# Kernel optimization log

Hardware: AMD Instinct MI355X
Metric: run time of the kernel (lower is better)

Reference implementation:

```python
import jax, jax.numpy as jnp
import numpy as np
from jax.scipy.special import gammaln

EPS = 1e-8
N_SAMPLES = 2 ** 17
ATTACK_FULL_SIZE = 2048
CPD = 16
N_RES = 16
EXPR = 2
N_OSC = 2
N_GAUSS = 8
N_EVENTS = 4
FRAMES = 128
DEF_FRAMES = 128
N_LEVELS = 11  # log2(ATTACK_FULL_SIZE)


def unit_norm(x, axis=-1):
    return x / (jnp.linalg.norm(x, axis=axis, keepdims=True) + EPS)


def fft_convolve(a, b):
    # zero-pad to 2n to avoid circular wraparound, multiply spectra, crop to n
    n = a.shape[-1]
    fa = jnp.fft.rfft(a, n=2 * n, axis=-1)
    fb = jnp.fft.rfft(b, n=2 * n, axis=-1)
    return jnp.fft.irfft(fa * fb, n=2 * n, axis=-1)[..., :n]


def upsample_with_holes(x, size):
    # zero-insertion upsampling: place frames at stride `factor`
    factor = size // x.shape[-1]
    out = jnp.zeros(x.shape[:-1] + (size,), x.dtype)
    return out.at[..., ::factor].set(x)


def interpolate_last_axis(x, size):
    # linear interpolation, align_corners=False semantics (torch F.interpolate)
    n = x.shape[-1]
    scale = n / size
    src = jnp.clip((jnp.arange(size) + 0.5) * scale - 0.5, 0.0, n - 1.0)
    lo = jnp.floor(src).astype(jnp.int32)
    hi = jnp.minimum(lo + 1, n - 1)
    w = (src - lo).astype(x.dtype)
    return x[..., lo] * (1.0 - w) + x[..., hi] * w


def ensure_last_axis_length(x, size):
    n = x.shape[-1]
    if n == size:
        return x
    if n > size:
        return x[..., :size]
    return jnp.pad(x, [(0, 0)] * (x.ndim - 1) + [(0, size - n)])


def sparse_softmax(x):
    # hard one-hot forward, softmax straight-through backward
    sm = jax.nn.softmax(x, axis=-1)
    hard = jax.nn.one_hot(jnp.argmax(x, axis=-1), x.shape[-1], dtype=x.dtype)
    return hard + sm - jax.lax.stop_gradient(sm)


def hierarchical_dirac(p):
    # p: (..., L, 2) binary choices per level -> one-hot dirac of length 2**L
    sel = sparse_softmax(p)
    sig = sel[..., 0, :]
    for i in range(1, p.shape[-2]):
        sig = (sig[..., :, None] * sel[..., i, :][..., None, :]).reshape(*sig.shape[:-1], -1)
    return sig


def gamma_pdf(mean, std, n_elements):
    # gamma pdf on support (eps, 1], parameterized by mean/std
    t = jnp.linspace(EPS, 1.0, n_elements)
    k = (mean / (std + EPS)) ** 2
    rate = mean / (std ** 2 + EPS)
    k = k[..., None]
    rate = rate[..., None]
    logp = k * jnp.log(rate + EPS) + (k - 1.0) * jnp.log(t) - rate * t - gammaln(k)
    return jnp.exp(logp)


def damped_harmonic_oscillator(time, mass, damping, tension, x0):
    # underdamped closed-form solution, v0 = 0
    omega0_sq = tension / mass
    gamma = damping / (2.0 * mass)
    omega = jnp.sqrt(omega0_sq - gamma ** 2)
    A = x0
    B = gamma * x0 / omega
    return jnp.exp(-gamma * time) * (A * jnp.cos(omega * time) + B * jnp.sin(omega * time))


def dho_block(damping, mass, tension, disp, amps, tmod=None, scaling=None):
    time = jnp.linspace(0.0, 10.0, N_SAMPLES).reshape(1, 1, 1, N_SAMPLES)
    t = tension[..., None]  # (N_OSC, N_RES, EXPR, 1)
    if tmod is not None:
        t = t + tmod[0] * scaling  # broadcast -> (N_OSC, N_RES, EXPR, N_SAMPLES)
    x = damped_harmonic_oscillator(
        time,
        jax.nn.sigmoid(mass[..., None]) * 2.0,
        jax.nn.sigmoid(damping[..., None]) * 30.0,
        10.0 ** t,
        disp[..., None],
    )
    x = (x * amps).sum(axis=0)  # sum over oscillators
    return x.reshape(1, 1, N_RES, EXPR, N_SAMPLES)


def attack_envelopes(means, stds, amps, pos, overall_amp):
    m, s, a = jnp.abs(means), jnp.abs(stds), jnp.abs(amps)
    p = hierarchical_dirac(pos)  # (1,1,CPD,NG,2048)
    x = gamma_pdf(m, s, ATTACK_FULL_SIZE) * a[..., None]
    x = fft_convolve(x, p)
    x = x.sum(axis=2)  # (1,1,NG,2048)
    x = unit_norm(x)
    x = x * overall_amp[..., None]  # broadcast -> (1,1,CPD,NG,2048)
    x = x.sum(axis=-2)  # (1,1,CPD,2048)
    return x.reshape(CPD, ATTACK_FULL_SIZE)


def _forward(control_signal, deformations, ae_means, ae_stds, ae_amps, ae_pos,
             ae_overall_amp, dho_damping, dho_mass, dho_tension, dho_disp, dho_amp,
             influences, stack_mix, router, layer_mix, gains, attack_noise):
    b, ne, cpd, frames = control_signal.shape
    # --- DampedHarmonicOscillatorStack ---
    o1 = dho_block(dho_damping[0], dho_mass[0], dho_tension[0], dho_disp[0], dho_amp[0])
    o2 = dho_block(dho_damping[1], dho_mass[1], dho_tension[1], dho_disp[1], dho_amp[1], o1, influences[0])
    o3 = dho_block(dho_damping[2], dho_mass[2], dho_tension[2], dho_disp[2], dho_amp[2], o2, influences[1])
    res = (jnp.stack([o1, o2, o3], axis=-1) * jax.nn.softmax(stack_mix, axis=-1)).sum(axis=-1)
    res = unit_norm(res)
    # --- AttackEnvelopes ---
    ae = attack_envelopes(ae_means, ae_stds, ae_amps, ae_pos, ae_overall_amp)
    # --- execute_layer ---
    routed = jnp.einsum('becf,cr->berf', control_signal, router)
    before = routed
    res = unit_norm(res)  # execute_layer normalizes again
    routed = upsample_with_holes(routed.reshape(b, ne, N_RES, 1, frames), N_SAMPLES)
    # ae.shape[-1] == window_size, so materialize_attack_envelopes just multiplies noise
    impulse = ensure_last_axis_length(ae * attack_noise, N_SAMPLES).reshape(1, 1, cpd, 1, N_SAMPLES)
    routed = fft_convolve(impulse, routed)  # (1,ne,N_RES,1,S)
    cs = routed.reshape(1, ne, cpd, N_SAMPLES).sum(axis=1, keepdims=True)
    conv = fft_convolve(routed, res)  # (1,ne,N_RES,EXPR,S)
    base = jnp.zeros_like(deformations).at[:, :, 0:1, :].set(1.0)
    d = jax.nn.softmax(base + deformations, axis=-2)
    d = interpolate_last_axis(d.reshape(b, 1, 1, EXPR, -1), N_SAMPLES)
    x = (d * conv).sum(axis=-2)  # (1,ne,N_RES,S)
    mixes = jax.nn.softmax(layer_mix.reshape(1, 1, N_RES, 1, 1, 2), axis=-1)
    stacked = jnp.stack([routed, x.reshape(routed.shape)], axis=-1)
    x = (mixes * stacked).sum(axis=-1)
    x = x.reshape(1, 1, N_RES, -1)
    summed = jnp.tanh(x * jnp.abs(gains.reshape(1, 1, N_RES, 1)))
    summed = summed.sum(axis=-2, keepdims=True)
    return summed, before, cs


def setup_inputs() -> dict:
    key = jax.random.key(0)
    ks = jax.random.split(key, 20)
    u = lambda k, shape, lo, hi: jax.random.uniform(k, shape, jnp.float32, lo, hi)
    inp = {}
    inp['control_signal'] = jax.random.uniform(ks[0], (1, N_EVENTS, CPD, FRAMES), jnp.float32)
    inp['deformations'] = jax.random.normal(ks[1], (1, 1, EXPR, DEF_FRAMES), jnp.float32)
    inp['ae_means'] = u(ks[2], (1, 1, CPD, N_GAUSS), -6.0, 6.0)
    inp['ae_stds'] = u(ks[3], (1, 1, CPD, N_GAUSS), 0.5, 6.0)
    inp['ae_amps'] = u(ks[4], (1, 1, CPD, N_GAUSS), -6.0, 6.0)
    inp['ae_pos'] = u(ks[5], (1, 1, CPD, N_GAUSS, N_LEVELS, 2), -1.0, 1.0)
    inp['ae_overall_amp'] = u(ks[6], (1, 1, CPD, 1), -1.0, 1.0)
    inp['dho_damping'] = u(ks[7], (3, N_OSC, N_RES, EXPR), 0.5, 1.5)
    inp['dho_mass'] = u(ks[8], (3, N_OSC, N_RES, EXPR), -2.0, 2.0)
    inp['dho_tension'] = u(ks[9], (3, N_OSC, N_RES, EXPR), 4.0, 9.0)
    inp['dho_disp'] = u(ks[10], (3, N_OSC, N_RES, EXPR), -1.0, 2.0)
    inp['dho_amp'] = u(ks[11], (3, N_OSC, N_RES, EXPR, 1), -1.0, 1.0)
    inp['influences'] = u(ks[12], (2, N_OSC, N_RES, EXPR, 1), -0.01, 0.01)
    inp['stack_mix'] = u(ks[13], (1, 1, N_RES, EXPR, 1, 3), -1.0, 1.0)
    router = u(ks[14], (CPD, N_RES), -1.0, 1.0)
    mask = (jax.random.uniform(ks[15], (CPD, N_RES)) < 0.1).astype(jnp.float32)
    inp['router'] = router * mask
    inp['layer_mix'] = u(ks[16], (N_RES, 2), -1.0, 1.0)
    inp['gains'] = u(ks[17], (N_RES, 1), 0.01, 1.1)
    inp['attack_noise'] = u(ks[18], (CPD, ATTACK_FULL_SIZE), -1.0, 1.0)
    return inp


def reference(control_signal, deformations, ae_means, ae_stds, ae_amps, ae_pos,
              ae_overall_amp, dho_damping, dho_mass, dho_tension, dho_disp, dho_amp,
              influences, stack_mix, router, layer_mix, gains, attack_noise):
    return _forward(control_signal, deformations, ae_means, ae_stds, ae_amps, ae_pos,
                    ae_overall_amp, dho_damping, dho_mass, dho_tension, dho_disp, dho_amp,
                    influences, stack_mix, router, layer_mix, gains, attack_noise)
```

## Files before the change

### kernel.cpp

```cpp
#include <hip/hip_runtime.h>
#include <math.h>

#define NS 131072
#define EPSF 1e-8f

#define OFF_IMP    8388608u
#define OFF_VG     8421376u
#define OFF_DW     8437760u
#define OFF_FV     8568832u
#define OFF_NORM   8577024u
#define OFF_MIX0   8577064u
#define OFF_MIX1   8577080u
#define OFF_GABS   8577096u
#define OFF_PART   8578560u
#define OFF_GSSP   8594944u
#define OFF_DHP    8595200u

#define AFRAG_USH  4194304u
#define ABF2_USH   4726784u
#define HB_USH     8388608u

typedef __attribute__((ext_vector_type(8))) short short8;
typedef __attribute__((ext_vector_type(4))) float floatx4;
typedef __attribute__((ext_vector_type(4))) unsigned short ushort4v;

#define INV2PI 0.15915494309189535f

__device__ __forceinline__ float sigmf(float x) { return 1.0f / (1.0f + expf(-x)); }

__device__ __forceinline__ unsigned short f2bf(float x) {
  unsigned u = __float_as_uint(x);
  unsigned r = (u + 0x7FFFu + ((u >> 16) & 1u)) >> 16;
  return (unsigned short)r;
}

__global__ __launch_bounds__(256) void k0_params(
    const float* __restrict__ ddmp, const float* __restrict__ dmas,
    const float* __restrict__ dten, const float* __restrict__ ddisp,
    const float* __restrict__ damp, const float* __restrict__ infl,
    const float* __restrict__ smix, float* __restrict__ wsf)
{
  int tid = threadIdx.x;
  int rx = tid >> 3, ent = tid & 7;
  int r = rx >> 1, x = rx & 1;
  float* g = wsf + OFF_DHP + rx * 40;
  if (ent < 6) {
    int bb = ent >> 1, o = ent & 1;
    int id = ((bb * 2 + o) * 16 + r) * 2 + x;
    float mass = 2.0f * sigmf(dmas[id]);
    float gam = 30.0f * sigmf(ddmp[id]) / (2.0f * mass);
    double W = exp((double)dten[id] * 2.302585092994046) / (double)mass;
    float x0v = ddisp[id];
    float ampv = damp[id];
    float infv = 0.f;
    if (bb == 1) infv = infl[(o * 16 + r) * 2 + x];
    if (bb == 2) infv = infl[((2 + o) * 16 + r) * 2 + x];
    g[0 + ent]  = -gam;
    g[6 + ent]  = ampv * x0v;
    g[12 + ent] = gam * ampv * x0v;
    g[18 + ent] = infv * 2.3025851f;
    if (bb == 0) {
      double om = sqrt(W - (double)gam * (double)gam);
      g[24 + o] = (float)((double)(gam * x0v * ampv) / om);
      g[26 + o] = (float)(om * 0.15915494309189535);
    } else {
      g[28 + ent - 2] = (float)W;
    }
    if (ent == 0) { g[32] = 0.f; g[36] = 0.f; g[37] = 0.f; g[38] = 0.f; g[39] = 0.f; }
  } else if (ent == 6) {
    float a0 = smix[rx * 3], a1 = smix[rx * 3 + 1], a2 = smix[rx * 3 + 2];
    float mm = fmaxf(a0, fmaxf(a1, a2));
    float e0 = expf(a0 - mm), e1 = expf(a1 - mm), e2 = expf(a2 - mm);
    float inv = 1.0f / (e0 + e1 + e2);
    g[33] = e0 * inv; g[34] = e1 * inv; g[35] = e2 * inv;
  }
}

__global__ __launch_bounds__(256) void k01_prep_dho(
    const float* __restrict__ csig, const float* __restrict__ deform,
    const float* __restrict__ smix_unused, const float* __restrict__ router,
    const float* __restrict__ lmix, const float* __restrict__ gains,
    const float* __restrict__ means, const float* __restrict__ stds,
    const float* __restrict__ amps, const float* __restrict__ pos,
    float* __restrict__ wsf, unsigned short* __restrict__ abf2,
    unsigned short* __restrict__ resb, float* __restrict__ partials,
    float* __restrict__ out)
{
  int tid = threadIdx.x;
  int bid = blockIdx.x;
  if (bid < 512) {
    int t = bid * 256 + tid;
    {
      float src = (t + 0.5f) * (1.0f / 1024.0f) - 0.5f;
      src = fminf(fmaxf(src, 0.0f), 127.0f);
      int lo = (int)src;
      int hi = min(lo + 1, 127);
      float w = src - (float)lo;
      float c0l = 1.0f / (1.0f + expf(deform[128 + lo] - (1.0f + deform[lo])));
      float c0h = 1.0f / (1.0f + expf(deform[128 + hi] - (1.0f + deform[hi])));
      wsf[OFF_DW + t] = c0l * (1.0f - w) + c0h * w;
    }
    int mt = bid & 7, e = (bid >> 3) & 3, r = (bid >> 5) & 15;
    __shared__ float fvrow[128];
    if (tid < 128) {
      float s = 0.f;
      for (int c = 0; c < 16; ++c)
        s += csig[(e * 16 + c) * 128 + tid] * router[c * 16 + r];
      fvrow[tid] = s;
      if (mt == 0) {
        wsf[OFF_FV + (e * 16 + r) * 128 + tid] = s;
        out[524288 + (e * 16 + r) * 128 + tid] = s;
      }
    }
    __syncthreads();
    {
      int gid = bid * 256 + tid;
      int lane = gid & 63;
      int kt = (gid >> 6) & 3;
      int m = lane & 15, quad = lane >> 4;
      int base = mt * 16 + m - kt * 32 - quad * 8;
      short8 v;
#pragma unroll
      for (int j = 0; j < 8; ++j) {
        int f = base - j;
        unsigned short b = 0;
        if (f >= 0 && f < 128) b = f2bf(fvrow[f]);
        v[j] = (short)b;
      }
      *(short8*)&abf2[(size_t)gid * 8] = v;
    }
    if (bid == 0 && tid < 16) {
      int r2 = tid;
      float l0 = lmix[r2 * 2], l1 = lmix[r2 * 2 + 1];
      float mx = fmaxf(l0, l1);
      float e0 = expf(l0 - mx), e1 = expf(l1 - mx), inv = 1.0f / (e0 + e1);
      wsf[OFF_MIX0 + r2] = e0 * inv;
      wsf[OFF_MIX1 + r2] = e1 * inv;
      wsf[OFF_GABS + r2] = fabsf(gains[r2]);
    }
  } else if (bid < 576) {
    int gb = bid - 512;
    int g = gb >> 3;
    int i = (gb & 7) * 256 + tid;
    __shared__ float kS[16], rateS[16], logAS[16], aS[16];
    __shared__ int dS[16];
    __shared__ float red[4];
    if (tid < 16) {
      int c = tid, idx = c * 8 + g;
      double m = fabs((double)means[idx]);
      double s = fabs((double)stds[idx]);
      double k = m / (s + 1e-8); k = k * k;
      double rate = m / (s * s + 1e-8);
      double logA = k * log(rate + 1e-8) - lgamma(k);
      kS[c] = (float)k; rateS[c] = (float)rate; logAS[c] = (float)logA;
      aS[c] = fabsf(amps[idx]);
      int d = 0;
      for (int l = 0; l < 11; ++l) {
        float p0 = pos[(idx * 11 + l) * 2], p1 = pos[(idx * 11 + l) * 2 + 1];
        d = d * 2 + (p1 > p0 ? 1 : 0);
      }
      dS[c] = d;
    }
    __syncthreads();
    const float step = (float)((1.0 - 1e-8) / 2047.0);
    float v = 0.f;
    for (int c = 0; c < 16; ++c) {
      int mi = i - dS[c];
      if (mi >= 0) {
        float tm = 1e-8f + (float)mi * step;
        float lp = logAS[c] + (kS[c] - 1.0f) * __logf(tm) - rateS[c] * tm;
        v += aS[c] * __expf(lp);
      }
    }
    wsf[OFF_VG + g * 2048 + i] = v;
    float sumsq = v * v;
#pragma unroll
    for (int off = 32; off; off >>= 1) sumsq += __shfl_down(sumsq, off, 64);
    if ((tid & 63) == 0) red[tid >> 6] = sumsq;
    __syncthreads();
    if (tid == 0) wsf[OFF_GSSP + gb] = red[0] + red[1] + red[2] + red[3];
  } else {
    int b = bid - 576;
    int rx = b >> 7;
    int t0 = (b & 127) * 1024 + tid * 4;
    __shared__ float pf[40];
    __shared__ float bred[4];
    if (tid < 40) pf[tid] = wsf[OFF_DHP + rx * 40 + tid];
    __syncthreads();
    float sqacc = 0.f;
    unsigned short h4[4];
#pragma unroll
    for (int u = 0; u < 4; ++u) {
      float ttf = (float)(t0 + u) * (10.0f / 131071.0f);
      float o1v = 0.f;
#pragma unroll
      for (int o = 0; o < 2; ++o) {
        float fr = pf[26 + o] * ttf;
        fr -= rintf(fr);
        float sn = __builtin_amdgcn_sinf(fr);
        float cn = __builtin_amdgcn_cosf(fr);
        float ex = __expf(pf[o] * ttf);
        o1v += ex * (pf[6 + o] * cn + pf[24 + o] * sn);
      }
      float prev = o1v, o2v = 0.f, o3v = 0.f;
#pragma unroll
      for (int blk = 1; blk < 3; ++blk) {
        float acc = 0.f;
#pragma unroll
        for (int oo = 0; oo < 2; ++oo) {
          int o = blk * 2 + oo;
          float ng = pf[o];
          float p10 = __expf(prev * pf[18 + o]);
          float rad = __builtin_fmaf(pf[28 + o - 2], p10, -(ng * ng));
          float om = __builtin_amdgcn_sqrtf(rad);
          float fr = (om * INV2PI) * ttf;
          fr -= rintf(fr);
          float sn = __builtin_amdgcn_sinf(fr);
          float cn = __builtin_amdgcn_cosf(fr);
          float Bp = pf[12 + o] * __builtin_amdgcn_rcpf(om);
          float ex = __expf(ng * ttf);
          acc += ex * (pf[6 + o] * cn + Bp * sn);
        }
        if (blk == 1) o2v = acc; else o3v = acc;
        prev = acc;
      }
      float rv = pf[33] * o1v + pf[34] * o2v + pf[35] * o3v;
      h4[u] = f2bf(rv);
      sqacc += rv * rv;
    }
    ushort4v hv;
    hv[0] = h4[0]; hv[1] = h4[1]; hv[2] = h4[2]; hv[3] = h4[3];
    *(ushort4v*)&resb[(size_t)rx * NS + t0] = hv;
#pragma unroll
    for (int off = 32; off; off >>= 1) sqacc += __shfl_down(sqacc, off, 64);
    if ((tid & 63) == 0) bred[tid >> 6] = sqacc;
    __syncthreads();
    if (tid == 0)
      partials[rx * 512 + (b & 127)] = bred[0] + bred[1] + bred[2] + bred[3];
  }
}

__global__ __launch_bounds__(256) void kB_mid(
    const float* __restrict__ ovamp, const float* __restrict__ noise,
    float* __restrict__ wsf, unsigned short* __restrict__ abf)
{
  int bid = blockIdx.x;
  int tid = threadIdx.x;
  if (bid < 32) {
    int rx = bid;
    const float* partials = wsf + OFF_PART;
    __shared__ float red[4];
    float s = (tid < 128) ? partials[rx * 512 + tid] : 0.f;
#pragma unroll
    for (int off = 32; off; off >>= 1) s += __shfl_down(s, off, 64);
    if ((tid & 63) == 0) red[tid >> 6] = s;
    __syncthreads();
    if (tid == 0) wsf[OFF_NORM + rx] = red[0] + red[1] + red[2] + red[3];
    return;
  }
  __shared__ float wS[8];
  if (tid < 8) {
    float g8 = 0.f;
#pragma unroll
    for (int u = 0; u < 8; ++u) g8 += wsf[OFF_GSSP + tid * 8 + u];
    wS[tid] = 1.0f / (sqrtf(g8) + EPSF);
  }
  __syncthreads();
  const float* vg = wsf + OFF_VG;
  if (bid < 160) {
    int idx0 = bid - 32;
    int c = idx0 >> 3;
    int i = (idx0 & 7) * 256 + tid;
    float S = 0.f;
#pragma unroll
    for (int g = 0; g < 8; ++g) S += vg[g * 2048 + i] * wS[g];
    wsf[OFF_IMP + c * 2048 + i] = ovamp[c] * S * noise[c * 2048 + i];
    return;
  }
  int gid = (bid - 160) * 256 + tid;
  if (gid >= 66560) return;
  int r = gid / (65 * 64);
  int rem = gid % (65 * 64);
  int sc = rem >> 6, lane = rem & 63;
  int m = lane & 15, quad = lane >> 4;
  int qp = (quad < 2) ? quad : quad - 4;
  int base = 32 * sc + m - 8 * qp;
  float oa = ovamp[r];
  short8 v;
#pragma unroll
  for (int j = 0; j < 8; ++j) {
    int idx = base - j;
    unsigned short b = 0;
    if (idx >= 0 && idx < 2048) {
      float S = 0.f;
#pragma unroll
      for (int g = 0; g < 8; ++g) S += vg[g * 2048 + idx] * wS[g];
      b = f2bf(oa * S * noise[r * 2048 + idx]);
    }
    v[j] = (short)b;
  }
  *(short8*)&abf[(size_t)gid * 8] = v;
}

__global__ __launch_bounds__(256) void k4_mfma(
    const unsigned short* __restrict__ resb, const unsigned short* __restrict__ abf,
    const float* __restrict__ wsf, unsigned short* __restrict__ Hb)
{
  int rx = blockIdx.y, r = rx >> 1;
  int n0 = blockIdx.x * 256;
  __shared__ __align__(16) unsigned short Xs[9280];
  int tid = threadIdx.x;
  for (int i = tid; i < 772; i += 256) {
    int q_rel = i >> 1, p8 = (i & 1) * 8;
    int q = n0 - 130 + q_rel;
    short8 v = {0, 0, 0, 0, 0, 0, 0, 0};
    if (q >= 0) v = *(const short8*)&resb[(size_t)rx * NS + q * 16 + p8];
    *(short8*)&Xs[q_rel * 24 + p8] = v;
  }
  __syncthreads();
  int lane = tid & 63, w = tid >> 6;
  int quad = lane >> 4, nl = lane & 15;
  float n1 = sqrtf(wsf[OFF_NORM + rx]);
  float s1 = 1.0f / (n1 + EPSF);
  float scale = s1 * (1.0f / (n1 * s1 + EPSF)) * wsf[OFF_MIX1 + r];
  const short8* af = (const short8*)(abf) + (size_t)r * 65 * 64 + lane;
  floatx4 acc0 = {0,0,0,0}, acc1 = {0,0,0,0}, acc2 = {0,0,0,0}, acc3 = {0,0,0,0};
  const char* xbase = (const char*)Xs + (size_t)(130 + w * 64 + nl - (quad >> 1)) * 48
                      + (quad & 1) * 16;
  short8 wbuf[25];
#pragma unroll
  for (int s = -24; s < 0; ++s)
    wbuf[s + 25] = *(const short8*)(xbase - 96 * s);
#pragma unroll
  for (int sc = 0; sc < 65; ++sc) {
    wbuf[sc % 25] = *(const short8*)(xbase - 96 * sc);
    short8 a = af[sc * 64];
    acc0 = __builtin_amdgcn_mfma_f32_16x16x32_bf16(a, wbuf[sc % 25],        acc0, 0, 0, 0);
    acc1 = __builtin_amdgcn_mfma_f32_16x16x32_bf16(a, wbuf[(sc + 17) % 25], acc1, 0, 0, 0);
    acc2 = __builtin_amdgcn_mfma_f32_16x16x32_bf16(a, wbuf[(sc + 9) % 25],  acc2, 0, 0, 0);
    acc3 = __builtin_amdgcn_mfma_f32_16x16x32_bf16(a, wbuf[(sc + 1) % 25],  acc3, 0, 0, 0);
  }
  unsigned short* hp = Hb + (size_t)rx * NS + 16 * (n0 + w * 64 + nl) + quad * 4;
  ushort4v h0, h1, h2, h3;
#pragma unroll
  for (int i = 0; i < 4; ++i) {
    h0[i] = f2bf(acc0[i] * scale);
    h1[i] = f2bf(acc1[i] * scale);
    h2[i] = f2bf(acc2[i] * scale);
    h3[i] = f2bf(acc3[i] * scale);
  }
  *(ushort4v*)(hp)       = h0;
  *(ushort4v*)(hp + 256) = h1;
  *(ushort4v*)(hp + 512) = h2;
  *(ushort4v*)(hp + 768) = h3;
}

__global__ __launch_bounds__(256) void k6_mfma(
    const unsigned short* __restrict__ Hb, const float* __restrict__ imp,
    const unsigned short* __restrict__ abf2,
    const float* __restrict__ wsf, float* __restrict__ out)
{
  int rm = blockIdx.y;
  int n0 = blockIdx.x * 16;
  int zz = blockIdx.z;
  int tid = threadIdx.x;
  int wm = tid >> 6, lane = tid & 63;
  int quad = lane >> 4, n = lane & 15;
  int col = n0 + n;
  int mt = zz * 4 + wm;

  __shared__ float fvs2[4][4][128];
  for (int i = tid; i < 2048; i += 256) {
    int rq = i >> 9, e = (i >> 7) & 3, q = i & 127;
    fvs2[rq][e][q] = wsf[OFF_FV + (e * 16 + rq * 4 + rm) * 128 + q];
  }
  __syncthreads();

  float d0r[4];
  const float* dwg = wsf + OFF_DW;
#pragma unroll
  for (int i = 0; i < 4; ++i) {
    int q = mt * 16 + quad * 4 + i;
    d0r[i] = dwg[q * 1024 + col];
  }

  float tansum[4] = {0.f, 0.f, 0.f, 0.f};
  const short8* af = (const short8*)abf2;

  for (int rq = 0; rq < 4; ++rq) {
    int r = rq * 4 + rm;
    short8 bf0[4], bf1[4];
    const unsigned short* H0 = Hb + (size_t)(2 * r) * NS + col;
    const unsigned short* H1 = Hb + (size_t)(2 * r + 1) * NS + col;
#pragma unroll
    for (int kt = 0; kt < 4; ++kt) {
#pragma unroll
      for (int j = 0; j < 8; ++j) {
        int p = kt * 32 + quad * 8 + j;
        bf0[kt][j] = (short)H0[(size_t)p * 1024];
        bf1[kt][j] = (short)H1[(size_t)p * 1024];
      }
    }
    float impA = imp[r * 2048 + col];
    float impB = imp[r * 2048 + 1024 + col];
    float mix0r = wsf[OFF_MIX0 + r];
    float csum[4] = {0.f, 0.f, 0.f, 0.f};

    for (int e = 0; e < 4; ++e) {
      float ge = wsf[OFF_GABS + 4 * e + rq];
      const short8* afe = af + ((size_t)(r * 4 + e) * 32) * 64 + lane;
      floatx4 acc0 = {0, 0, 0, 0}, acc1 = {0, 0, 0, 0};
#pragma unroll
      for (int kt = 0; kt < 4; ++kt) {
        short8 a = afe[(mt * 4 + kt) * 64];
        acc0 = __builtin_amdgcn_mfma_f32_16x16x32_bf16(a, bf0[kt], acc0, 0, 0, 0);
        acc1 = __builtin_amdgcn_mfma_f32_16x16x32_bf16(a, bf1[kt], acc1, 0, 0, 0);
      }
#pragma unroll
      for (int i = 0; i < 4; ++i) {
        int q = mt * 16 + quad * 4 + i;
        float fq = fvs2[rq][e][q];
        float fqm = (q > 0) ? fvs2[rq][e][q - 1] : 0.f;
        float rsv = fq * impA + fqm * impB;
        csum[i] += rsv;
        float d0 = d0r[i];
        float conv = d0 * acc0[i] + (1.0f - d0) * acc1[i];
        float z = (mix0r * rsv + conv) * ge;
        float e2 = __expf(2.0f * z);
        tansum[i] += 1.0f - 2.0f * __builtin_amdgcn_rcpf(e2 + 1.0f);
      }
    }
#pragma unroll
    for (int i = 0; i < 4; ++i) {
      int q = mt * 16 + quad * 4 + i;
      out[532480 + (size_t)r * NS + q * 1024 + col] = csum[i];
    }
  }
#pragma unroll
  for (int i = 0; i < 4; ++i) {
    int q = mt * 16 + quad * 4 + i;
    out[(size_t)rm * NS + q * 1024 + col] = tansum[i];
  }
}

extern "C" void kernel_launch(void* const* d_in, const int* in_sizes, int n_in,
                              void* d_out, int out_size, void* d_ws, size_t ws_size,
                              hipStream_t stream) {
  const float* csig   = (const float*)d_in[0];
  const float* deform = (const float*)d_in[1];
  const float* aem    = (const float*)d_in[2];
  const float* aes    = (const float*)d_in[3];
  const float* aea    = (const float*)d_in[4];
  const float* aep    = (const float*)d_in[5];
  const float* aeo    = (const float*)d_in[6];
  const float* ddmp   = (const float*)d_in[7];
  const float* dmas   = (const float*)d_in[8];
  const float* dten   = (const float*)d_in[9];
  const float* ddisp  = (const float*)d_in[10];
  const float* damp   = (const float*)d_in[11];
  const float* infl   = (const float*)d_in[12];
  const float* smix   = (const float*)d_in[13];
  const float* router = (const float*)d_in[14];
  const float* lmix   = (const float*)d_in[15];
  const float* gains  = (const float*)d_in[16];
  const float* anoise = (const float*)d_in[17];

  float*  wsf = (float*)d_ws;
  unsigned short* resb = (unsigned short*)d_ws;
  unsigned short* abf  = (unsigned short*)d_ws + AFRAG_USH;
  unsigned short* abf2 = (unsigned short*)d_ws + ABF2_USH;
  unsigned short* Hb   = (unsigned short*)d_ws + HB_USH;
  float*  out = (float*)d_out;

  k0_params<<<1, 256, 0, stream>>>(ddmp, dmas, dten, ddisp, damp, infl, smix, wsf);
  k01_prep_dho<<<4672, 256, 0, stream>>>(csig, deform, smix, router, lmix, gains,
                                         aem, aes, aea, aep, wsf, abf2, resb,
                                         wsf + OFF_PART, out);
  kB_mid<<<420, 256, 0, stream>>>(aeo, anoise, wsf, abf);
  k4_mfma<<<dim3(32, 32), 256, 0, stream>>>(resb, abf, wsf, Hb);
  k6_mfma<<<dim3(64, 4, 2), 256, 0, stream>>>(Hb, wsf + OFF_IMP, abf2, wsf, out);
}
```

Baseline: 163.0 us.

## Use rotation recurrence for DHO oscillators, 8 samples per thread, vectorize attack frags

Each thread in the DHO phase of the prep kernel now computes 8 consecutive samples instead of 4. The fixed-frequency first oscillator's sin/cos and all damping exponentials are advanced by multiplying with per-step rotation and decay factors precomputed in the params kernel, so per-sample transcendentals are no longer needed for those terms. Block count and the partials reduction are adjusted to match. The bf16 attack-fragment builder in kB_mid gains a fast path that does vectorized unaligned float4 loads for interior indices. The recurrence can accumulate float rounding drift over the 8 steps.

Result: no change. 161.8 us, median of 2 (-0.7%).

```diff
diff --git a/kernel.cpp b/kernel.cpp
--- a/kernel.cpp
+++ b/kernel.cpp
@@ -23,6 +23,7 @@
 typedef __attribute__((ext_vector_type(8))) short short8;
 typedef __attribute__((ext_vector_type(4))) float floatx4;
 typedef __attribute__((ext_vector_type(4))) unsigned short ushort4v;
+typedef __attribute__((ext_vector_type(4), aligned(4))) float float4u;
 
 #define INV2PI 0.15915494309189535f
 
@@ -43,7 +44,8 @@
   int tid = threadIdx.x;
   int rx = tid >> 3, ent = tid & 7;
   int r = rx >> 1, x = rx & 1;
-  float* g = wsf + OFF_DHP + rx * 40;
+  float* g = wsf + OFF_DHP + rx * 48;
+  const double dtd = 10.0 / 131071.0;
   if (ent < 6) {
     int bb = ent >> 1, o = ent & 1;
     int id = ((bb * 2 + o) * 16 + r) * 2 + x;
@@ -59,14 +61,17 @@
     g[6 + ent]  = ampv * x0v;
     g[12 + ent] = gam * ampv * x0v;
     g[18 + ent] = infv * 2.3025851f;
+    g[40 + ent] = (float)exp(-(double)gam * dtd);
     if (bb == 0) {
       double om = sqrt(W - (double)gam * (double)gam);
       g[24 + o] = (float)((double)(gam * x0v * ampv) / om);
       g[26 + o] = (float)(om * 0.15915494309189535);
+      g[36 + o] = (float)sin(om * dtd);
+      g[38 + o] = (float)cos(om * dtd);
     } else {
       g[28 + ent - 2] = (float)W;
     }
-    if (ent == 0) { g[32] = 0.f; g[36] = 0.f; g[37] = 0.f; g[38] = 0.f; g[39] = 0.f; }
+    if (ent == 0) { g[32] = 0.f; g[46] = 0.f; g[47] = 0.f; }
   } else if (ent == 6) {
     float a0 = smix[rx * 3], a1 = smix[rx * 3 + 1], a2 = smix[rx * 3 + 2];
     float mm = fmaxf(a0, fmaxf(a1, a2));
@@ -181,27 +186,34 @@
     if (tid == 0) wsf[OFF_GSSP + gb] = red[0] + red[1] + red[2] + red[3];
   } else {
     int b = bid - 576;
-    int rx = b >> 7;
-    int t0 = (b & 127) * 1024 + tid * 4;
-    __shared__ float pf[40];
+    int rx = b >> 6;
+    int t0 = (b & 63) * 2048 + tid * 8;
+    __shared__ float pf[48];
     __shared__ float bred[4];
-    if (tid < 40) pf[tid] = wsf[OFF_DHP + rx * 40 + tid];
+    if (tid < 48) pf[tid] = wsf[OFF_DHP + rx * 48 + tid];
     __syncthreads();
+    const float dtf = 10.0f / 131071.0f;
+    float sn1[2], cn1[2], ex1[2], exd[4];
+    {
+      float ttf0 = (float)t0 * dtf;
+#pragma unroll
+      for (int o = 0; o < 2; ++o) {
+        float fr = pf[26 + o] * ttf0;
+        fr -= rintf(fr);
+        sn1[o] = __builtin_amdgcn_sinf(fr);
+        cn1[o] = __builtin_amdgcn_cosf(fr);
+        ex1[o] = __expf(pf[o] * ttf0);
+      }
+#pragma unroll
+      for (int oi = 0; oi < 4; ++oi) exd[oi] = __expf(pf[2 + oi] * ttf0);
+    }
     float sqacc = 0.f;
-    unsigned short h4[4];
-#pragma unroll
-    for (int u = 0; u < 4; ++u) {
-      float ttf = (float)(t0 + u) * (10.0f / 131071.0f);
-      float o1v = 0.f;
-#pragma unroll
-      for (int o = 0; o < 2; ++o) {
-        float fr = pf[26 + o] * ttf;
-        fr -= rintf(fr);
-        float sn = __builtin_amdgcn_sinf(fr);
-        float cn = __builtin_amdgcn_cosf(fr);
-        float ex = __expf(pf[o] * ttf);
-        o1v += ex * (pf[6 + o] * cn + pf[24 + o] * sn);
-      }
+    unsigned short h8[8];
+#pragma unroll
+    for (int u = 0; u < 8; ++u) {
+      float ttf = (float)(t0 + u) * dtf;
+      float o1v = ex1[0] * (pf[6] * cn1[0] + pf[24] * sn1[0])
+                + ex1[1] * (pf[7] * cn1[1] + pf[25] * sn1[1]);
       float prev = o1v, o2v = 0.f, o3v = 0.f;
 #pragma unroll
       for (int blk = 1; blk < 3; ++blk) {
@@ -218,25 +230,34 @@
           float sn = __builtin_amdgcn_sinf(fr);
           float cn = __builtin_amdgcn_cosf(fr);
           float Bp = pf[12 + o] * __builtin_amdgcn_rcpf(om);
-          float ex = __expf(ng * ttf);
-          acc += ex * (pf[6 + o] * cn + Bp * sn);
+          acc += exd[o - 2] * (pf[6 + o] * cn + Bp * sn);
         }
         if (blk == 1) o2v = acc; else o3v = acc;
         prev = acc;
       }
       float rv = pf[33] * o1v + pf[34] * o2v + pf[35] * o3v;
-      h4[u] = f2bf(rv);
+      h8[u] = f2bf(rv);
       sqacc += rv * rv;
-    }
-    ushort4v hv;
-    hv[0] = h4[0]; hv[1] = h4[1]; hv[2] = h4[2]; hv[3] = h4[3];
-    *(ushort4v*)&resb[(size_t)rx * NS + t0] = hv;
+#pragma unroll
+      for (int o = 0; o < 2; ++o) {
+        float ns = sn1[o] * pf[38 + o] + cn1[o] * pf[36 + o];
+        float nc = cn1[o] * pf[38 + o] - sn1[o] * pf[36 + o];
+        sn1[o] = ns; cn1[o] = nc;
+        ex1[o] *= pf[40 + o];
+      }
+#pragma unroll
+      for (int oi = 0; oi < 4; ++oi) exd[oi] *= pf[42 + oi];
+    }
+    short8 hv;
+#pragma unroll
+    for (int u = 0; u < 8; ++u) hv[u] = (short)h8[u];
+    *(short8*)&resb[(size_t)rx * NS + t0] = hv;
 #pragma unroll
     for (int off = 32; off; off >>= 1) sqacc += __shfl_down(sqacc, off, 64);
     if ((tid & 63) == 0) bred[tid >> 6] = sqacc;
     __syncthreads();
     if (tid == 0)
-      partials[rx * 512 + (b & 127)] = bred[0] + bred[1] + bred[2] + bred[3];
+      partials[rx * 512 + (b & 63)] = bred[0] + bred[1] + bred[2] + bred[3];
   }
 }
 
@@ -250,7 +271,7 @@
     int rx = bid;
     const float* partials = wsf + OFF_PART;
     __shared__ float red[4];
-    float s = (tid < 128) ? partials[rx * 512 + tid] : 0.f;
+    float s = (tid < 64) ? partials[rx * 512 + tid] : 0.f;
 #pragma unroll
     for (int off = 32; off; off >>= 1) s += __shfl_down(s, off, 64);
     if ((tid & 63) == 0) red[tid >> 6] = s;
@@ -287,17 +308,43 @@
   int base = 32 * sc + m - 8 * qp;
   float oa = ovamp[r];
   short8 v;
-#pragma unroll
-  for (int j = 0; j < 8; ++j) {
-    int idx = base - j;
-    unsigned short b = 0;
-    if (idx >= 0 && idx < 2048) {
-      float S = 0.f;
-#pragma unroll
-      for (int g = 0; g < 8; ++g) S += vg[g * 2048 + idx] * wS[g];
-      b = f2bf(oa * S * noise[r * 2048 + idx]);
-    }
-    v[j] = (short)b;
+  if (base >= 7 && base < 2048) {
+    float S0 = 0.f, S1 = 0.f, S2 = 0.f, S3 = 0.f, S4 = 0.f, S5 = 0.f, S6 = 0.f, S7 = 0.f;
+#pragma unroll
+    for (int g = 0; g < 8; ++g) {
+      const float* p = vg + g * 2048 + (base - 7);
+      float4u a = *(const float4u*)p;
+      float4u b2 = *(const float4u*)(p + 4);
+      float wg = wS[g];
+      S7 = fmaf(a[0], wg, S7);  S6 = fmaf(a[1], wg, S6);
+      S5 = fmaf(a[2], wg, S5);  S4 = fmaf(a[3], wg, S4);
+      S3 = fmaf(b2[0], wg, S3); S2 = fmaf(b2[1], wg, S2);
+      S1 = fmaf(b2[2], wg, S1); S0 = fmaf(b2[3], wg, S0);
+    }
+    const float* np = noise + r * 2048 + (base - 7);
+    float4u na = *(const float4u*)np;
+    float4u nb = *(const float4u*)(np + 4);
+    v[0] = (short)f2bf(oa * S0 * nb[3]);
+    v[1] = (short)f2bf(oa * S1 * nb[2]);
+    v[2] = (short)f2bf(oa * S2 * nb[1]);
+    v[3] = (short)f2bf(oa * S3 * nb[0]);
+    v[4] = (short)f2bf(oa * S4 * na[3]);
+    v[5] = (short)f2bf(oa * S5 * na[2]);
+    v[6] = (short)f2bf(oa * S6 * na[1]);
+    v[7] = (short)f2bf(oa * S7 * na[0]);
+  } else {
+#pragma unroll
+    for (int j = 0; j < 8; ++j) {
+      int idx = base - j;
+      unsigned short b = 0;
+      if (idx >= 0 && idx < 2048) {
+        float S = 0.f;
+#pragma unroll
+        for (int g = 0; g < 8; ++g) S += vg[g * 2048 + idx] * wS[g];
+        b = f2bf(oa * S * noise[r * 2048 + idx]);
+      }
+      v[j] = (short)b;
+    }
   }
   *(short8*)&abf[(size_t)gid * 8] = v;
 }
@@ -473,7 +520,7 @@
   float*  out = (float*)d_out;
 
   k0_params<<<1, 256, 0, stream>>>(ddmp, dmas, dten, ddisp, damp, infl, smix, wsf);
-  k01_prep_dho<<<4672, 256, 0, stream>>>(csig, deform, smix, router, lmix, gains,
+  k01_prep_dho<<<2624, 256, 0, stream>>>(csig, deform, smix, router, lmix, gains,
                                          aem, aes, aea, aep, wsf, abf2, resb,
                                          wsf + OFF_PART, out);
   kB_mid<<<420, 256, 0, stream>>>(aeo, anoise, wsf, abf);
```
